# Optimization experiments

Measured on AMD Instinct MI355X. Metric: run time of the kernel, lower is better.

## Reference

```python
import jax, jax.numpy as jnp
import numpy as np

N_ENT = 100000
N_USR = 1024
E = 400000
D = 128
H = 4
R = 32


def setup_inputs() -> dict:
    key = jax.random.key(0)
    ks = jax.random.split(key, 9)
    a = float(np.sqrt(6.0 / (D + D)))  # xavier_uniform bound for [D, D]
    return {
        "entity_emb": jax.random.normal(ks[0], (N_ENT, D), dtype=jnp.float32),
        "user_emb": jax.random.normal(ks[1], (N_USR, D), dtype=jnp.float32),
        "interact_mat": jnp.zeros((1,), dtype=jnp.float32),  # unused by forward
        "weight": jax.random.normal(ks[2], (R, D), dtype=jnp.float32) * 0.1,
        "qTrans": jax.random.uniform(ks[3], (D, D), minval=-a, maxval=a, dtype=jnp.float32),
        "kTrans": jax.random.uniform(ks[4], (D, D), minval=-a, maxval=a, dtype=jnp.float32),
        "vTrans": jax.random.uniform(ks[5], (D, D), minval=-a, maxval=a, dtype=jnp.float32),
        "edge_index": jax.random.randint(ks[6], (2, E), 0, N_ENT, dtype=jnp.int64)
            if jax.config.jax_enable_x64 else jax.random.randint(ks[6], (2, E), 0, N_ENT, dtype=jnp.int32),
        "edge_type": jax.random.randint(ks[7], (E,), 1, R + 1, dtype=jnp.int32),  # types in [1, R]
        "layer": 0,
    }


def _kglayer(rows, col_embeds, embeds, n_seg, qT, kT, vT):
    # rows: [E] target-node index, col_embeds: [E, D] edge messages
    dh = D // H
    row_embeds = embeds[rows]                              # gather [E, D]
    q = (row_embeds @ qT).reshape(-1, H, dh)
    k = (col_embeds @ kT).reshape(-1, H, dh)
    v = (col_embeds @ vT).reshape(-1, H, dh)
    att = jnp.clip(jnp.einsum("ehd,ehd->eh", q, k), -10.0, 10.0)
    exp_att = jnp.exp(att)                                 # [E, H]
    att_norm = jax.ops.segment_sum(exp_att, rows, num_segments=n_seg)[rows]
    att = exp_att / (att_norm + 1e-8)
    res = (att[..., None] * v).reshape(-1, D)              # [E, D]
    return jax.ops.segment_sum(res, rows, num_segments=n_seg)


def _sim_hrt(head_emb, tail_emb, rel_emb):
    # per-edge scalar attention logit [E, 1]
    tr = jnp.linalg.norm(tail_emb * rel_emb, axis=1, keepdims=True)
    hr = jnp.linalg.norm(head_emb * rel_emb, axis=1, keepdims=True)
    return (hr * tr) ** 2


def reference(entity_emb, user_emb, interact_mat, weight, qTrans, kTrans, vTrans,
              edge_index, edge_type, layer):
    n_entities = entity_emb.shape[0]
    head, tail = edge_index[0], edge_index[1]
    rel = weight[edge_type - 1]                            # [E, D]
    neigh = entity_emb[tail] * rel                         # [E, D]
    kg_emb = _kglayer(head, neigh, entity_emb, n_entities, qTrans, kTrans, vTrans)
    w = _sim_hrt(kg_emb[head], kg_emb[tail], rel)          # [E, 1]
    w = jnp.broadcast_to(w, neigh.shape)                   # expand to [E, D]
    # scatter_softmax over edges sharing the same head (numerically stable)
    m = jax.ops.segment_max(w, head, num_segments=n_entities)[head]
    e = jnp.exp(w - m)
    s = jax.ops.segment_sum(e, head, num_segments=n_entities)[head]
    soft = e / s
    msg = soft * entity_emb[tail]
    return jax.ops.segment_sum(msg, head, num_segments=n_entities)
```

## Files before the change

kernel.cpp:

```cpp
#include <hip/hip_runtime.h>
#include <cstdint>

#define D 128
#define H 4
#define N_ENT 100000
#define N_EDGE 400000
#define R 32

#define SCAN_NB ((N_ENT + 511) / 512)

__global__ void k_hist(const int* __restrict__ head, int* __restrict__ deg) {
  const int e = blockIdx.x * 256 + threadIdx.x;
  if (e < N_EDGE) atomicAdd(&deg[head[e]], 1);
}

__global__ __launch_bounds__(256) void k_scan1(const int* __restrict__ deg,
                                               int* __restrict__ bsum) {
  const int t = threadIdx.x;
  const int i = blockIdx.x * 512 + t * 2;
  int v0 = (i < N_ENT) ? deg[i] : 0;
  int v1 = (i + 1 < N_ENT) ? deg[i + 1] : 0;
  int s = v0 + v1;
#pragma unroll
  for (int k = 1; k < 64; k <<= 1) s += __shfl_xor(s, k);
  __shared__ int ws[4];
  if ((t & 63) == 0) ws[t >> 6] = s;
  __syncthreads();
  if (t == 0) bsum[blockIdx.x] = ws[0] + ws[1] + ws[2] + ws[3];
}

__global__ __launch_bounds__(256) void k_scan2(const int* __restrict__ bsum,
                                               int* __restrict__ bbase,
                                               int* __restrict__ off) {
  __shared__ int sh[256];
  const int t = threadIdx.x;
  const int v = (t < SCAN_NB) ? bsum[t] : 0;
  sh[t] = v;
  __syncthreads();
  for (int d = 1; d < 256; d <<= 1) {
    const int u = (t >= d) ? sh[t - d] : 0;
    __syncthreads();
    sh[t] += u;
    __syncthreads();
  }
  if (t < SCAN_NB) bbase[t] = sh[t] - v;
  if (t == SCAN_NB - 1) off[N_ENT] = sh[t];
}

__global__ __launch_bounds__(256) void k_scan3(const int* __restrict__ deg,
                                               const int* __restrict__ bbase,
                                               int* __restrict__ off,
                                               int* __restrict__ cur) {
  __shared__ int sh[256];
  const int t = threadIdx.x;
  const int i = blockIdx.x * 512 + t * 2;
  const int v0 = (i < N_ENT) ? deg[i] : 0;
  const int v1 = (i + 1 < N_ENT) ? deg[i + 1] : 0;
  const int s = v0 + v1;
  sh[t] = s;
  __syncthreads();
  for (int d = 1; d < 256; d <<= 1) {
    const int u = (t >= d) ? sh[t - d] : 0;
    __syncthreads();
    sh[t] += u;
    __syncthreads();
  }
  const int ex = sh[t] - s + bbase[blockIdx.x];
  if (i < N_ENT) {
    off[i] = ex;
    cur[i] = ex;
  }
  if (i + 1 < N_ENT) {
    off[i + 1] = ex + v0;
    cur[i + 1] = ex + v0;
  }
}

__global__ void k_scatter(const int* __restrict__ head,
                          const int* __restrict__ tail,
                          const int* __restrict__ etype, int* __restrict__ cur,
                          int2* __restrict__ teP) {
  const int e = blockIdx.x * 256 + threadIdx.x;
  if (e >= N_EDGE) return;
  const int hd = head[e];
  const int pos = atomicAdd(&cur[hd], 1);
  teP[pos] = make_int2(tail[e], etype[e] - 1);
}

__global__ __launch_bounds__(256) void k_prep(const float* __restrict__ kT,
                                              float* __restrict__ kTt,
                                              const float* __restrict__ wrel,
                                              float* __restrict__ wrel2) {
  if (blockIdx.x < 16) {
    __shared__ float tile[32][33];
    const int bx = blockIdx.x & 3, by = blockIdx.x >> 2;
    const int c = threadIdx.x & 31;
    const int r0 = (threadIdx.x >> 5) * 4;
#pragma unroll
    for (int i = 0; i < 4; ++i)
      tile[r0 + i][c] = kT[(by * 32 + r0 + i) * 128 + bx * 32 + c];
    __syncthreads();
#pragma unroll
    for (int i = 0; i < 4; ++i)
      kTt[(bx * 32 + r0 + i) * 128 + by * 32 + c] = tile[c][r0 + i];
  } else {
    const int t = threadIdx.x;
#pragma unroll
    for (int s = 0; s < 4; ++s) {
      const int idx = (s * 256 + t) * 4;
      float4 v = *(const float4*)&wrel[idx];
      v.x *= v.x; v.y *= v.y; v.z *= v.z; v.w *= v.w;
      *(float4*)&wrel2[idx] = v;
    }
  }
}

__global__ __launch_bounds__(512) void k_qproj(const float* __restrict__ ent,
                                               const float* __restrict__ qT,
                                               float* __restrict__ Q) {
  __shared__ float sT[D * D];
  __shared__ float rows[D * 128];
  const int t = threadIdx.x;
  const int n0 = blockIdx.x * 128;
#pragma unroll
  for (int s = 0; s < 8; ++s) {
    const int idx = (s * 512 + t) * 4;
    *(float4*)&sT[idx] = *(const float4*)&qT[idx];
  }
  {
    const int g = t & 3;
    const int n = t >> 2;
    const int node = n0 + n;
    if (node < N_ENT) {
      const float* src = ent + (size_t)node * D;
#pragma unroll
      for (int s = 0; s < 8; ++s) {
        const int i = s * 16 + g * 4;
        float4 v = *(const float4*)&src[i];
        rows[(i + 0) * 128 + n] = v.x;
        rows[(i + 1) * 128 + n] = v.y;
        rows[(i + 2) * 128 + n] = v.z;
        rows[(i + 3) * 128 + n] = v.w;
      }
    } else {
#pragma unroll
      for (int s = 0; s < 8; ++s) {
        const int i = s * 16 + g * 4;
        rows[(i + 0) * 128 + n] = 0.f;
        rows[(i + 1) * 128 + n] = 0.f;
        rows[(i + 2) * 128 + n] = 0.f;
        rows[(i + 3) * 128 + n] = 0.f;
      }
    }
  }
  __syncthreads();
  const int jj = t & 15;
  const int ee = t >> 4;
  float acc[4][8];
#pragma unroll
  for (int a = 0; a < 4; ++a)
#pragma unroll
    for (int b = 0; b < 8; ++b) acc[a][b] = 0.f;
#pragma unroll 4
  for (int i = 0; i < D; ++i) {
    float4 b0 = *(float4*)&sT[i * D + jj * 8];
    float4 b1 = *(float4*)&sT[i * D + jj * 8 + 4];
    float4 a0 = *(float4*)&rows[i * 128 + ee * 4];
    float bv[8] = {b0.x, b0.y, b0.z, b0.w, b1.x, b1.y, b1.z, b1.w};
    float av[4] = {a0.x, a0.y, a0.z, a0.w};
#pragma unroll
    for (int a = 0; a < 4; ++a)
#pragma unroll
      for (int b = 0; b < 8; ++b) acc[a][b] = fmaf(av[a], bv[b], acc[a][b]);
  }
#pragma unroll
  for (int a = 0; a < 4; ++a) {
    const int node = n0 + ee * 4 + a;
    if (node < N_ENT) {
      float4 o0 = {acc[a][0], acc[a][1], acc[a][2], acc[a][3]};
      float4 o1 = {acc[a][4], acc[a][5], acc[a][6], acc[a][7]};
      *(float4*)&Q[(size_t)node * D + jj * 8] = o0;
      *(float4*)&Q[(size_t)node * D + jj * 8 + 4] = o1;
    }
  }
}

__global__ __launch_bounds__(256, 4) void k_fused(
    const float* __restrict__ ent, const float* __restrict__ wrel,
    const float* __restrict__ kTt, const float* __restrict__ vT,
    const float* __restrict__ wrel2, const float* __restrict__ qkg,
    float* __restrict__ S, const int* __restrict__ off,
    const int2* __restrict__ teP) {
  __shared__ float sQ[8 * 128];
  __shared__ float sPA[8 * 512];
  __shared__ float sW[R * D];
  const int t = threadIdx.x;
  const int base = blockIdx.x * 8;
  const int wid = t >> 6;
  const int half = (t >> 5) & 1;
  const int l32 = t & 31;
  const int kk = wid * 2 + half;
  const int n = base + kk;

  {
    const int k = t >> 5;
    const int c4 = (t & 31) * 4;
    *(float4*)&sQ[k * 128 + c4] =
        *(const float4*)&qkg[(size_t)(base + k) * D + c4];
#pragma unroll
    for (int s = 0; s < 4; ++s) {
      const int i4 = (s * 256 + t) * 4;
      *(float4*)&sW[i4] = *(const float4*)&wrel[i4];
    }
  }

  const int eb = off[n];
  const int deg = off[n + 1] - eb;
  int2 pfc = make_int2(0, 0), pfn = make_int2(0, 0);
  float4 xv = {0, 0, 0, 0};
  if (deg > 0) {
    pfc = teP[eb];
    xv = *(const float4*)&ent[(size_t)pfc.x * D + l32 * 4];
  }
  if (deg > 1) pfn = teP[eb + 1];
  __syncthreads();

  {
    const int i = t & 127;
    const int sub = t >> 7;
    float pp[2][8];
#pragma unroll
    for (int hh = 0; hh < 2; ++hh)
#pragma unroll
      for (int k = 0; k < 8; ++k) pp[hh][k] = 0.f;
#pragma unroll
    for (int hh = 0; hh < 2; ++hh) {
      const int h = sub * 2 + hh;
#pragma unroll 2
      for (int c4 = 0; c4 < 8; ++c4) {
        const float kv0 = kTt[(h * 32 + c4 * 4 + 0) * 128 + i];
        const float kv1 = kTt[(h * 32 + c4 * 4 + 1) * 128 + i];
        const float kv2 = kTt[(h * 32 + c4 * 4 + 2) * 128 + i];
        const float kv3 = kTt[(h * 32 + c4 * 4 + 3) * 128 + i];
#pragma unroll
        for (int k = 0; k < 8; ++k) {
          const float4 q = *(const float4*)&sQ[k * 128 + h * 32 + c4 * 4];
          pp[hh][k] = fmaf(kv0, q.x, pp[hh][k]);
          pp[hh][k] = fmaf(kv1, q.y, pp[hh][k]);
          pp[hh][k] = fmaf(kv2, q.z, pp[hh][k]);
          pp[hh][k] = fmaf(kv3, q.w, pp[hh][k]);
        }
      }
    }
#pragma unroll
    for (int hh = 0; hh < 2; ++hh)
#pragma unroll
      for (int k = 0; k < 8; ++k)
        sPA[k * 512 + (sub * 2 + hh) * 128 + i] = pp[hh][k];
  }
  __syncthreads();

  {
    const int lp = l32 & 3;
    const float4 P0 = *(const float4*)&sPA[kk * 512 + 0 * 128 + l32 * 4];
    const float4 P1 = *(const float4*)&sPA[kk * 512 + 1 * 128 + l32 * 4];
    const float4 P2 = *(const float4*)&sPA[kk * 512 + 2 * 128 + l32 * 4];
    const float4 P3 = *(const float4*)&sPA[kk * 512 + 3 * 128 + l32 * 4];
    float4 rv = {0, 0, 0, 0};
    if (deg > 0) rv = *(const float4*)&sW[pfc.y * 128 + l32 * 4];
    float4 b0 = {0, 0, 0, 0}, b1 = {0, 0, 0, 0};
    float4 b2 = {0, 0, 0, 0}, b3 = {0, 0, 0, 0};
    float s0 = 0.f, s1 = 0.f, s2 = 0.f, s3 = 0.f;
    for (int idx = 0; idx < deg; ++idx) {
      const float4 nh = {xv.x * rv.x, xv.y * rv.y, xv.z * rv.z, xv.w * rv.w};
      if (idx + 1 < deg) {
        xv = *(const float4*)&ent[(size_t)pfn.x * D + l32 * 4];
        rv = *(const float4*)&sW[pfn.y * 128 + l32 * 4];
      }
      if (idx + 2 < deg) pfn = teP[eb + idx + 2];
      float d0 = nh.x * P0.x + nh.y * P0.y + nh.z * P0.z + nh.w * P0.w;
      float d1 = nh.x * P1.x + nh.y * P1.y + nh.z * P1.z + nh.w * P1.w;
      float d2 = nh.x * P2.x + nh.y * P2.y + nh.z * P2.z + nh.w * P2.w;
      float d3 = nh.x * P3.x + nh.y * P3.y + nh.z * P3.z + nh.w * P3.w;
      float x01 = (l32 & 1) ? d1 : d0;
      float y01 = (l32 & 1) ? d0 : d1;
      x01 += __shfl_xor(y01, 1);
      float x23 = (l32 & 1) ? d3 : d2;
      float y23 = (l32 & 1) ? d2 : d3;
      x23 += __shfl_xor(y23, 1);
      float xa = (l32 & 2) ? x23 : x01;
      float xb = (l32 & 2) ? x01 : x23;
      xa += __shfl_xor(xb, 2);
      xa += __shfl_xor(xa, 4);
      xa += __shfl_xor(xa, 8);
      xa += __shfl_xor(xa, 16);
      const float eL = __expf(fminf(fmaxf(xa, -10.f), 10.f));
      const float e0 = eL;
      const float e1 = __shfl_xor(eL, 1);
      const float e2 = __shfl_xor(eL, 2);
      const float e3 = __shfl_xor(eL, 3);
      b0.x = fmaf(e0, nh.x, b0.x); b0.y = fmaf(e0, nh.y, b0.y);
      b0.z = fmaf(e0, nh.z, b0.z); b0.w = fmaf(e0, nh.w, b0.w);
      b1.x = fmaf(e1, nh.x, b1.x); b1.y = fmaf(e1, nh.y, b1.y);
      b1.z = fmaf(e1, nh.z, b1.z); b1.w = fmaf(e1, nh.w, b1.w);
      b2.x = fmaf(e2, nh.x, b2.x); b2.y = fmaf(e2, nh.y, b2.y);
      b2.z = fmaf(e2, nh.z, b2.z); b2.w = fmaf(e2, nh.w, b2.w);
      b3.x = fmaf(e3, nh.x, b3.x); b3.y = fmaf(e3, nh.y, b3.y);
      b3.z = fmaf(e3, nh.z, b3.z); b3.w = fmaf(e3, nh.w, b3.w);
      s0 += e0; s1 += e1; s2 += e2; s3 += e3;
    }
    const float i0 = 1.f / (s0 + 1e-8f);
    const float i1 = 1.f / (s1 + 1e-8f);
    const float i2 = 1.f / (s2 + 1e-8f);
    const float i3 = 1.f / (s3 + 1e-8f);
    float4 o0 = {b0.x * i0, b0.y * i0, b0.z * i0, b0.w * i0};
    float4 o1 = {b1.x * i1, b1.y * i1, b1.z * i1, b1.w * i1};
    float4 o2 = {b2.x * i2, b2.y * i2, b2.z * i2, b2.w * i2};
    float4 o3 = {b3.x * i3, b3.y * i3, b3.z * i3, b3.w * i3};
    const int sb = kk * 512 + l32 * 4;
    *(float4*)&sPA[sb + ((lp ^ 0) << 7)] = o0;
    *(float4*)&sPA[sb + ((lp ^ 1) << 7)] = o1;
    *(float4*)&sPA[sb + ((lp ^ 2) << 7)] = o2;
    *(float4*)&sPA[sb + ((lp ^ 3) << 7)] = o3;
  }
  __syncthreads();

  {
    const int c = t & 127;
    const int g4 = (t >> 7) * 4;
    const int h = c >> 5;
    float acc0 = 0.f, acc1 = 0.f, acc2 = 0.f, acc3 = 0.f;
    const float* agg0 = &sPA[(g4 + 0) * 512 + h * 128];
    const float* agg1 = &sPA[(g4 + 1) * 512 + h * 128];
    const float* agg2 = &sPA[(g4 + 2) * 512 + h * 128];
    const float* agg3 = &sPA[(g4 + 3) * 512 + h * 128];
#pragma unroll 4
    for (int d4 = 0; d4 < 32; ++d4) {
      const float4 a0 = *(const float4*)&agg0[d4 * 4];
      const float4 a1 = *(const float4*)&agg1[d4 * 4];
      const float4 a2 = *(const float4*)&agg2[d4 * 4];
      const float4 a3 = *(const float4*)&agg3[d4 * 4];
      const float v0 = vT[(d4 * 4 + 0) * 128 + c];
      const float v1 = vT[(d4 * 4 + 1) * 128 + c];
      const float v2 = vT[(d4 * 4 + 2) * 128 + c];
      const float v3 = vT[(d4 * 4 + 3) * 128 + c];
      acc0 = fmaf(a0.x, v0, acc0); acc0 = fmaf(a0.y, v1, acc0);
      acc0 = fmaf(a0.z, v2, acc0); acc0 = fmaf(a0.w, v3, acc0);
      acc1 = fmaf(a1.x, v0, acc1); acc1 = fmaf(a1.y, v1, acc1);
      acc1 = fmaf(a1.z, v2, acc1); acc1 = fmaf(a1.w, v3, acc1);
      acc2 = fmaf(a2.x, v0, acc2); acc2 = fmaf(a2.y, v1, acc2);
      acc2 = fmaf(a2.z, v2, acc2); acc2 = fmaf(a2.w, v3, acc2);
      acc3 = fmaf(a3.x, v0, acc3); acc3 = fmaf(a3.y, v1, acc3);
      acc3 = fmaf(a3.z, v2, acc3); acc3 = fmaf(a3.w, v3, acc3);
    }
    sQ[(g4 + 0) * 128 + c] = acc0 * acc0;
    sQ[(g4 + 1) * 128 + c] = acc1 * acc1;
    sQ[(g4 + 2) * 128 + c] = acc2 * acc2;
    sQ[(g4 + 3) * 128 + c] = acc3 * acc3;
  }
  __syncthreads();

  {
    const int nn = t >> 5;
    const int r = t & 31;
    const float* kg2 = &sQ[nn * 128];
    const float* w2 = &wrel2[r * 128];
    float acc = 0.f;
#pragma unroll 4
    for (int c4 = 0; c4 < 32; ++c4) {
      const float4 a = *(const float4*)&kg2[c4 * 4];
      const float4 b = *(const float4*)&w2[c4 * 4];
      acc = fmaf(a.x, b.x, acc); acc = fmaf(a.y, b.y, acc);
      acc = fmaf(a.z, b.z, acc); acc = fmaf(a.w, b.w, acc);
    }
    S[(size_t)(base + nn) * 32 + r] = acc;
  }
}

__global__ __launch_bounds__(256) void k_out2(
    const float* __restrict__ ent, const float* __restrict__ S,
    const int* __restrict__ off, const int2* __restrict__ teP,
    float* __restrict__ out) {
  const int t = threadIdx.x;
  const int wid = t >> 6;
  const int half = (t >> 5) & 1;
  const int l32 = t & 31;
  const int kk = wid * 2 + half;
  const int n = blockIdx.x * 8 + kk;
  if (n >= N_ENT) return;
  const int eb = off[n];
  const int deg = off[n + 1] - eb;
  const float sn = S[(size_t)n * 32 + l32];
  float4 acc = {0, 0, 0, 0};
  float m = 0.f, ssum = 0.f;
  for (int b = 0; b < deg; b += 32) {
    const int idx = b + l32;
    const bool val = idx < deg;
    const int e = eb + (val ? idx : 0);
    const int2 tp = teP[e];
    const int tl = tp.x;
    const int ty = tp.y;
    const float snv = __shfl(sn, ty, 32);
    float w = val ? snv * S[(size_t)tl * 32 + ty] : -1.f;
    float cm = w;
#pragma unroll
    for (int k = 1; k < 32; k <<= 1) cm = fmaxf(cm, __shfl_xor(cm, k));
    const float mnew = fmaxf(m, cm);
    const float scale = __expf(m - mnew);
    const float el = val ? __expf(w - mnew) : 0.f;
    float cs = el;
#pragma unroll
    for (int k = 1; k < 32; k <<= 1) cs += __shfl_xor(cs, k);
    ssum = ssum * scale + cs;
    acc.x *= scale; acc.y *= scale; acc.z *= scale; acc.w *= scale;
    const int cnt = (deg - b < 32) ? deg - b : 32;
    for (int j0 = 0; j0 < cnt; j0 += 4) {
      const int rem = cnt - j0;
      const int t0 = __shfl(tl, j0 + 0, 32);
      float4 r0 = *(const float4*)&ent[(size_t)t0 * D + l32 * 4];
      float4 r1, r2, r3;
      if (rem > 1) {
        const int t1 = __shfl(tl, j0 + 1, 32);
        r1 = *(const float4*)&ent[(size_t)t1 * D + l32 * 4];
      }
      if (rem > 2) {
        const int t2 = __shfl(tl, j0 + 2, 32);
        r2 = *(const float4*)&ent[(size_t)t2 * D + l32 * 4];
      }
      if (rem > 3) {
        const int t3 = __shfl(tl, j0 + 3, 32);
        r3 = *(const float4*)&ent[(size_t)t3 * D + l32 * 4];
      }
      const float w0 = __shfl(el, j0 + 0, 32);
      acc.x = fmaf(w0, r0.x, acc.x); acc.y = fmaf(w0, r0.y, acc.y);
      acc.z = fmaf(w0, r0.z, acc.z); acc.w = fmaf(w0, r0.w, acc.w);
      if (rem > 1) {
        const float w1 = __shfl(el, j0 + 1, 32);
        acc.x = fmaf(w1, r1.x, acc.x); acc.y = fmaf(w1, r1.y, acc.y);
        acc.z = fmaf(w1, r1.z, acc.z); acc.w = fmaf(w1, r1.w, acc.w);
      }
      if (rem > 2) {
        const float w2 = __shfl(el, j0 + 2, 32);
        acc.x = fmaf(w2, r2.x, acc.x); acc.y = fmaf(w2, r2.y, acc.y);
        acc.z = fmaf(w2, r2.z, acc.z); acc.w = fmaf(w2, r2.w, acc.w);
      }
      if (rem > 3) {
        const float w3 = __shfl(el, j0 + 3, 32);
        acc.x = fmaf(w3, r3.x, acc.x); acc.y = fmaf(w3, r3.y, acc.y);
        acc.z = fmaf(w3, r3.z, acc.z); acc.w = fmaf(w3, r3.w, acc.w);
      }
    }
    m = mnew;
  }
  const float inv = (deg > 0) ? 1.f / ssum : 0.f;
  float4 o = {acc.x * inv, acc.y * inv, acc.z * inv, acc.w * inv};
  *(float4*)&out[(size_t)n * D + l32 * 4] = o;
}

extern "C" void kernel_launch(void* const* d_in, const int* in_sizes, int n_in,
                              void* d_out, int out_size, void* d_ws,
                              size_t ws_size, hipStream_t stream) {
  const float* ent = (const float*)d_in[0];
  const float* wrel = (const float*)d_in[3];
  const float* qT = (const float*)d_in[4];
  const float* kT = (const float*)d_in[5];
  const float* vT = (const float*)d_in[6];
  const int* eidx = (const int*)d_in[7];
  const int* etype = (const int*)d_in[8];
  const int* head = eidx;
  const int* tail = eidx + N_EDGE;

  float* S = (float*)d_ws;
  int* off = (int*)(S + (size_t)N_ENT * 32);
  int* cur = off + (N_ENT + 2);
  int* deg = cur + N_ENT;
  int* bsum = deg + N_ENT;
  int* bbase = bsum + SCAN_NB;
  int2* teP = (int2*)(bbase + SCAN_NB);
  float* kTt = (float*)(teP + N_EDGE);
  float* wrel2 = (float*)cur;
  float* qkg = (float*)d_out;

  hipMemsetAsync(deg, 0, N_ENT * sizeof(int), stream);
  k_hist<<<(N_EDGE + 255) / 256, 256, 0, stream>>>(head, deg);
  k_scan1<<<SCAN_NB, 256, 0, stream>>>(deg, bsum);
  k_scan2<<<1, 256, 0, stream>>>(bsum, bbase, off);
  k_scan3<<<SCAN_NB, 256, 0, stream>>>(deg, bbase, off, cur);
  k_scatter<<<(N_EDGE + 255) / 256, 256, 0, stream>>>(head, tail, etype, cur,
                                                      teP);
  k_prep<<<17, 256, 0, stream>>>(kT, kTt, wrel, wrel2);
  k_qproj<<<(N_ENT + 127) / 128, 512, 0, stream>>>(ent, qT, qkg);
  k_fused<<<N_ENT / 8, 256, 0, stream>>>(ent, wrel, kTt, vT, wrel2, qkg, S,
                                         off, teP);
  k_out2<<<(N_ENT + 7) / 8, 256, 0, stream>>>(ent, S, off, teP, qkg);
}
```

Before: 554.2 us.

## Drop shared relation table in fused kernel and raise occupancy target

```diff
diff --git a/kernel.cpp b/kernel.cpp
--- a/kernel.cpp
+++ b/kernel.cpp
@@ -87,32 +87,19 @@
   teP[pos] = make_int2(tail[e], etype[e] - 1);
 }
 
-__global__ __launch_bounds__(256) void k_prep(const float* __restrict__ kT,
-                                              float* __restrict__ kTt,
-                                              const float* __restrict__ wrel,
-                                              float* __restrict__ wrel2) {
-  if (blockIdx.x < 16) {
-    __shared__ float tile[32][33];
-    const int bx = blockIdx.x & 3, by = blockIdx.x >> 2;
-    const int c = threadIdx.x & 31;
-    const int r0 = (threadIdx.x >> 5) * 4;
-#pragma unroll
-    for (int i = 0; i < 4; ++i)
-      tile[r0 + i][c] = kT[(by * 32 + r0 + i) * 128 + bx * 32 + c];
-    __syncthreads();
-#pragma unroll
-    for (int i = 0; i < 4; ++i)
-      kTt[(bx * 32 + r0 + i) * 128 + by * 32 + c] = tile[c][r0 + i];
-  } else {
-    const int t = threadIdx.x;
-#pragma unroll
-    for (int s = 0; s < 4; ++s) {
-      const int idx = (s * 256 + t) * 4;
-      float4 v = *(const float4*)&wrel[idx];
-      v.x *= v.x; v.y *= v.y; v.z *= v.z; v.w *= v.w;
-      *(float4*)&wrel2[idx] = v;
-    }
-  }
+__global__ __launch_bounds__(256) void k_tr(const float* __restrict__ in,
+                                            float* __restrict__ out) {
+  __shared__ float tile[32][33];
+  const int bx = blockIdx.x & 3, by = blockIdx.x >> 2;
+  const int c = threadIdx.x & 31;
+  const int r0 = (threadIdx.x >> 5) * 4;
+#pragma unroll
+  for (int i = 0; i < 4; ++i)
+    tile[r0 + i][c] = in[(by * 32 + r0 + i) * 128 + bx * 32 + c];
+  __syncthreads();
+#pragma unroll
+  for (int i = 0; i < 4; ++i)
+    out[(bx * 32 + r0 + i) * 128 + by * 32 + c] = tile[c][r0 + i];
 }
 
 __global__ __launch_bounds__(512) void k_qproj(const float* __restrict__ ent,
@@ -185,17 +172,16 @@
   }
 }
 
-__global__ __launch_bounds__(256, 4) void k_fused(
+__global__ __launch_bounds__(256, 8) void k_fused(
     const float* __restrict__ ent, const float* __restrict__ wrel,
     const float* __restrict__ kTt, const float* __restrict__ vT,
-    const float* __restrict__ wrel2, const float* __restrict__ qkg,
-    float* __restrict__ S, const int* __restrict__ off,
-    const int2* __restrict__ teP) {
+    const float* __restrict__ qkg, float* __restrict__ S,
+    const int* __restrict__ off, const int2* __restrict__ teP) {
   __shared__ float sQ[8 * 128];
   __shared__ float sPA[8 * 512];
-  __shared__ float sW[R * D];
   const int t = threadIdx.x;
   const int base = blockIdx.x * 8;
+
   const int wid = t >> 6;
   const int half = (t >> 5) & 1;
   const int l32 = t & 31;
@@ -207,22 +193,16 @@
     const int c4 = (t & 31) * 4;
     *(float4*)&sQ[k * 128 + c4] =
         *(const float4*)&qkg[(size_t)(base + k) * D + c4];
-#pragma unroll
-    for (int s = 0; s < 4; ++s) {
-      const int i4 = (s * 256 + t) * 4;
-      *(float4*)&sW[i4] = *(const float4*)&wrel[i4];
-    }
   }
 
   const int eb = off[n];
   const int deg = off[n + 1] - eb;
-  int2 pfc = make_int2(0, 0), pfn = make_int2(0, 0);
-  float4 xv = {0, 0, 0, 0};
+  float4 xv = {0, 0, 0, 0}, rv = {0, 0, 0, 0};
   if (deg > 0) {
-    pfc = teP[eb];
-    xv = *(const float4*)&ent[(size_t)pfc.x * D + l32 * 4];
-  }
-  if (deg > 1) pfn = teP[eb + 1];
+    const int2 pf = teP[eb];
+    xv = *(const float4*)&ent[(size_t)pf.x * D + l32 * 4];
+    rv = *(const float4*)&wrel[(size_t)pf.y * D + l32 * 4];
+  }
   __syncthreads();
 
   {
@@ -266,18 +246,17 @@
     const float4 P1 = *(const float4*)&sPA[kk * 512 + 1 * 128 + l32 * 4];
     const float4 P2 = *(const float4*)&sPA[kk * 512 + 2 * 128 + l32 * 4];
     const float4 P3 = *(const float4*)&sPA[kk * 512 + 3 * 128 + l32 * 4];
-    float4 rv = {0, 0, 0, 0};
-    if (deg > 0) rv = *(const float4*)&sW[pfc.y * 128 + l32 * 4];
     float4 b0 = {0, 0, 0, 0}, b1 = {0, 0, 0, 0};
     float4 b2 = {0, 0, 0, 0}, b3 = {0, 0, 0, 0};
     float s0 = 0.f, s1 = 0.f, s2 = 0.f, s3 = 0.f;
     for (int idx = 0; idx < deg; ++idx) {
-      const float4 nh = {xv.x * rv.x, xv.y * rv.y, xv.z * rv.z, xv.w * rv.w};
+      const float4 cx = xv, cr = rv;
       if (idx + 1 < deg) {
-        xv = *(const float4*)&ent[(size_t)pfn.x * D + l32 * 4];
-        rv = *(const float4*)&sW[pfn.y * 128 + l32 * 4];
-      }
-      if (idx + 2 < deg) pfn = teP[eb + idx + 2];
+        const int2 pf = teP[eb + idx + 1];
+        xv = *(const float4*)&ent[(size_t)pf.x * D + l32 * 4];
+        rv = *(const float4*)&wrel[(size_t)pf.y * D + l32 * 4];
+      }
+      const float4 nh = {cx.x * cr.x, cx.y * cr.y, cx.z * cr.z, cx.w * cr.w};
       float d0 = nh.x * P0.x + nh.y * P0.y + nh.z * P0.z + nh.w * P0.w;
       float d1 = nh.x * P1.x + nh.y * P1.y + nh.z * P1.z + nh.w * P1.w;
       float d2 = nh.x * P2.x + nh.y * P2.y + nh.z * P2.z + nh.w * P2.w;
@@ -353,6 +332,7 @@
       acc3 = fmaf(a3.x, v0, acc3); acc3 = fmaf(a3.y, v1, acc3);
       acc3 = fmaf(a3.z, v2, acc3); acc3 = fmaf(a3.w, v3, acc3);
     }
+    __syncthreads();
     sQ[(g4 + 0) * 128 + c] = acc0 * acc0;
     sQ[(g4 + 1) * 128 + c] = acc1 * acc1;
     sQ[(g4 + 2) * 128 + c] = acc2 * acc2;
@@ -364,14 +344,16 @@
     const int nn = t >> 5;
     const int r = t & 31;
     const float* kg2 = &sQ[nn * 128];
-    const float* w2 = &wrel2[r * 128];
+    const float* w = &wrel[(size_t)r * 128];
     float acc = 0.f;
 #pragma unroll 4
     for (int c4 = 0; c4 < 32; ++c4) {
       const float4 a = *(const float4*)&kg2[c4 * 4];
-      const float4 b = *(const float4*)&w2[c4 * 4];
-      acc = fmaf(a.x, b.x, acc); acc = fmaf(a.y, b.y, acc);
-      acc = fmaf(a.z, b.z, acc); acc = fmaf(a.w, b.w, acc);
+      const float4 b = *(const float4*)&w[c4 * 4];
+      acc = fmaf(a.x, b.x * b.x, acc);
+      acc = fmaf(a.y, b.y * b.y, acc);
+      acc = fmaf(a.z, b.z * b.z, acc);
+      acc = fmaf(a.w, b.w * b.w, acc);
     }
     S[(size_t)(base + nn) * 32 + r] = acc;
   }
@@ -478,7 +460,6 @@
   int* bbase = bsum + SCAN_NB;
   int2* teP = (int2*)(bbase + SCAN_NB);
   float* kTt = (float*)(teP + N_EDGE);
-  float* wrel2 = (float*)cur;
   float* qkg = (float*)d_out;
 
   hipMemsetAsync(deg, 0, N_ENT * sizeof(int), stream);
@@ -488,9 +469,9 @@
   k_scan3<<<SCAN_NB, 256, 0, stream>>>(deg, bbase, off, cur);
   k_scatter<<<(N_EDGE + 255) / 256, 256, 0, stream>>>(head, tail, etype, cur,
                                                       teP);
-  k_prep<<<17, 256, 0, stream>>>(kT, kTt, wrel, wrel2);
+  k_tr<<<16, 256, 0, stream>>>(kT, kTt);
   k_qproj<<<(N_ENT + 127) / 128, 512, 0, stream>>>(ent, qT, qkg);
-  k_fused<<<N_ENT / 8, 256, 0, stream>>>(ent, wrel, kTt, vT, wrel2, qkg, S,
-                                         off, teP);
+  k_fused<<<N_ENT / 8, 256, 0, stream>>>(ent, wrel, kTt, vT, qkg, S, off,
+                                         teP);
   k_out2<<<(N_ENT + 7) / 8, 256, 0, stream>>>(ent, S, off, teP, qkg);
 }
```

Result: slower. 640.8 us (+15.6%).
